# Performance work log

Measured on AMD Instinct MI355X. Metric: run time of the kernel, lower is better.

Reference implementation:

```python
import jax, jax.numpy as jnp
import numpy as np

N, XDIM, D, K = 400000, 128, 3, 4
TWO_PI = 2.0 * np.pi


def _scaled(k, shape):
    fan_in = shape[0]
    return jax.random.normal(k, shape, jnp.float32) * np.float32(1.0 / np.sqrt(fan_in))


def setup_inputs() -> dict:
    key = jax.random.key(0)
    ks = jax.random.split(key, 9)
    return {
        "x1": jax.random.normal(ks[0], (N, XDIM), jnp.float32),
        "enc_w1": _scaled(ks[1], (XDIM, 16)), "enc_b1": jnp.zeros((16,), jnp.float32),
        "enc_w2": _scaled(ks[2], (16, 8)),   "enc_b2": jnp.zeros((8,), jnp.float32),
        "enc_w3": _scaled(ks[3], (8, 1)),    "enc_b3": jnp.zeros((1,), jnp.float32),
        "dec_w1": _scaled(ks[4], (1, 8)),    "dec_b1": jnp.zeros((8,), jnp.float32),
        "dec_w2": _scaled(ks[5], (8, 16)),   "dec_b2": jnp.zeros((16,), jnp.float32),
        "dec_w3": _scaled(ks[6], (16, XDIM)),"dec_b3": jnp.zeros((XDIM,), jnp.float32),
        "est_w1": _scaled(ks[7], (D, 8)),    "est_b1": jnp.zeros((8,), jnp.float32),
        "est_w2": _scaled(ks[8], (8, K)),    "est_b2": jnp.zeros((K,), jnp.float32),
    }


def reference(x1, enc_w1, enc_b1, enc_w2, enc_b2, enc_w3, enc_b3,
              dec_w1, dec_b1, dec_w2, dec_b2, dec_w3, dec_b3,
              est_w1, est_b1, est_w2, est_b2):
    # encoder: Dense(16,tanh)->Dense(8,tanh)->Dense(1,tanh)
    h = jnp.tanh(x1 @ enc_w1 + enc_b1)
    h = jnp.tanh(h @ enc_w2 + enc_b2)
    z1 = jnp.tanh(h @ enc_w3 + enc_b3)            # [N,1]
    # decoder: Dense(8,tanh)->Dense(16,tanh)->Dense(xdim, linear)
    h = jnp.tanh(z1 @ dec_w1 + dec_b1)
    h = jnp.tanh(h @ dec_w2 + dec_b2)
    x2 = h @ dec_w3 + dec_b3                      # [N,xdim]

    # relative distances
    dist_cos = jnp.sum(x1 * x2, axis=1, keepdims=True) / (
        jnp.linalg.norm(x1, axis=1, keepdims=True) * jnp.linalg.norm(x2, axis=1, keepdims=True))
    dist_euc = jnp.linalg.norm(x1 - x2, axis=1, keepdims=True)
    z = jnp.concatenate([z1, dist_cos, dist_euc], axis=1)   # [N,D]

    # estimator: Dense(8,tanh)->Dense(K,softmax)
    gamma = jax.nn.softmax(jnp.tanh(z @ est_w1 + est_b1) @ est_w2 + est_b2)  # [N,K]

    # GMM parameters from soft assignments
    gamma_sum = jnp.sum(gamma, axis=0)                        # [K]
    phi = jnp.mean(gamma, axis=0)                             # [K]
    mu = jnp.einsum('ik,il->kl', gamma, z) / gamma_sum[:, None]          # [K,D]
    z_centered = jnp.sqrt(gamma)[:, :, None] * (z[:, None, :] - mu[None, :, :])  # [N,K,D]
    sigma = jnp.einsum('ikl,ikm->klm', z_centered, z_centered) / gamma_sum[:, None, None]  # [K,D,D]

    # per-sample energy
    z_mu = z[:, None, :] - mu[None, :, :]                     # [N,K,D]
    sigma_inv = jnp.linalg.inv(sigma)                         # [K,D,D]
    item1 = jnp.log(phi)[None, :]                             # [1,K]
    item2 = -0.5 * jnp.einsum('nkd,kde,nke->nk', z_mu, sigma_inv, z_mu)  # [N,K]
    sigma_det = jnp.linalg.det(TWO_PI * sigma)                # [K]
    item3 = jnp.log(jnp.sqrt(sigma_det))[None, :]             # [1,K]
    energy = -jnp.sum(item1 + item2 - item3, axis=1)          # [N]

    # loss
    lambda1, lambda2 = 0.01, 0.0001
    diag = jnp.diagonal(sigma, axis1=-2, axis2=-1)            # [K,D]
    loss3 = lambda2 * jnp.sum(1.0 / diag)
    loss2 = lambda1 * jnp.mean(energy)
    loss1 = jnp.mean(jnp.sum(jnp.square(x1 - x2), axis=1))
    loss = loss1 + loss2 + loss3
    return energy, loss
```

## Files before the change

kernel.cpp:

```cpp
#include <hip/hip_runtime.h>

#define NSAMP 400000
#define NBLK  1563


__device__ __forceinline__ float ftanh(float x) {
    float e = __expf(2.0f * x);
    return 1.0f - __fdividef(2.0f, e + 1.0f);
}

__global__ __launch_bounds__(256) void prep_kernel(const float* __restrict__ dw3,
                                                   const float* __restrict__ db3,
                                                   float* __restrict__ Gm,
                                                   float* __restrict__ gv,
                                                   float* __restrict__ bb) {
    __shared__ float sw3[2048];
    __shared__ float sb3[128];
    int t = threadIdx.x;
    for (int k = t; k < 2048; k += 256) sw3[k] = dw3[k];
    if (t < 128) sb3[t] = db3[t];
    __syncthreads();
    int a = t >> 4, b = t & 15;
    float s = 0.f;
    for (int j = 0; j < 128; ++j) s = fmaf(sw3[a * 128 + j], sw3[b * 128 + j], s);
    Gm[t] = s;
    if (t < 16) {
        float sg = 0.f;
        for (int j = 0; j < 128; ++j) sg = fmaf(sw3[t * 128 + j], sb3[j], sg);
        gv[t] = sg;
    }
    if (t == 0) {
        float sbv = 0.f;
        for (int j = 0; j < 128; ++j) sbv = fmaf(sb3[j], sb3[j], sbv);
        *bb = sbv;
    }
}

__global__ __launch_bounds__(256) void pass1_kernel(
    const float* __restrict__ x1,
    const float* __restrict__ ew1, const float* __restrict__ eb1,
    const float* __restrict__ ew2, const float* __restrict__ eb2,
    const float* __restrict__ ew3, const float* __restrict__ eb3,
    const float* __restrict__ dw1, const float* __restrict__ db1,
    const float* __restrict__ dw2, const float* __restrict__ db2,
    const float* __restrict__ dw3, const float* __restrict__ db3,
    const float* __restrict__ tw1, const float* __restrict__ tb1,
    const float* __restrict__ tw2, const float* __restrict__ tb2,
    const float* __restrict__ Gm, const float* __restrict__ gv,
    const float* __restrict__ bbp,
    double* __restrict__ acc, float4* __restrict__ zbuf) {
    __shared__ float4 lbuf[2048];
    __shared__ float sPart[4][41];
    __shared__ __align__(16) float sEw1[2048];
    __shared__ __align__(16) float sDw3[2048];
    __shared__ __align__(16) float sGm[256];
    __shared__ __align__(16) float sDb3[128];
    __shared__ __align__(16) float sEw2[128];
    __shared__ __align__(16) float sDw2[128];
    __shared__ __align__(16) float sTw1[24];
    __shared__ __align__(16) float sTw2[32];
    __shared__ float sGv[16], sEb1[16], sDb2[16];
    __shared__ float sEb2[8], sEw3[8], sDw1[8], sDb1[8], sTb1[8];
    __shared__ float sTb2[4];
    __shared__ float sBb, sEb3;

    int t = threadIdx.x;
    int i = blockIdx.x * 256 + t;
    bool active = (i < NSAMP);
    int bbase = blockIdx.x * 256;
    int w = t >> 6, lane = t & 63;
    int sw2 = (t >> 1) & 3;
    const float4* x1f4 = (const float4*)x1;

    const float4* p[4];
#pragma unroll
    for (int c2 = 0; c2 < 4; ++c2) {
        int idx = (w * 4 + c2) * 64 + lane;
        int row = idx >> 2, qs = idx & 3;
        int q = qs ^ ((row >> 1) & 3);
        int grow = bbase + row;
        if (grow >= NSAMP) grow = NSAMP - 1;
        p[c2] = x1f4 + (size_t)grow * 32 + q;
    }
#pragma unroll
    for (int c2 = 0; c2 < 4; ++c2) {
        __builtin_amdgcn_global_load_lds(
            (const __attribute__((address_space(1))) void*)p[c2],
            (__attribute__((address_space(3))) void*)(lbuf + (w * 4 + c2) * 64),
            16, 0, 0);
        p[c2] += 4;
    }

    for (int k = t; k < 2048; k += 256) { sEw1[k] = ew1[k]; sDw3[k] = dw3[k]; }
    sGm[t & 255] = Gm[t & 255];
    if (t < 128) { sDb3[t] = db3[t]; sEw2[t] = ew2[t]; sDw2[t] = dw2[t]; }
    if (t < 16) { sGv[t] = gv[t]; sEb1[t] = eb1[t]; sDb2[t] = db2[t]; }
    if (t < 8) { sEb2[t] = eb2[t]; sEw3[t] = ew3[t]; sDw1[t] = dw1[t];
                 sDb1[t] = db1[t]; sTb1[t] = tb1[t]; }
    if (t < 24) sTw1[t] = tw1[t];
    if (t < 32) sTw2[t] = tw2[t];
    if (t < 4) sTb2[t] = tb2[t];
    if (t == 0) { sBb = *bbp; sEb3 = eb3[0]; }
    __syncthreads();

    const float4* sEw1_4 = (const float4*)sEw1;
    const float4* sDw3_4 = (const float4*)sDw3;
    const float4* sDb3_4 = (const float4*)sDb3;
    const float4* sGm_4  = (const float4*)sGm;
    const float4* sEw2_4 = (const float4*)sEw2;
    const float4* sDw2_4 = (const float4*)sDw2;
    const float4* sTw1_4 = (const float4*)sTw1;
    const float4* sTw2_4 = (const float4*)sTw2;

    float u[16], v[16];
#pragma unroll
    for (int k = 0; k < 16; ++k) { u[k] = 0.f; v[k] = 0.f; }
    float s2 = 0.f, sb = 0.f;

    auto consume = [&](int blk, int bofs) {
        float xe[16];
#pragma unroll
        for (int q = 0; q < 4; ++q) {
            float4 w4 = lbuf[bofs + t * 4 + (q ^ sw2)];
            xe[q * 4 + 0] = w4.x; xe[q * 4 + 1] = w4.y;
            xe[q * 4 + 2] = w4.z; xe[q * 4 + 3] = w4.w;
        }
        int j0 = blk * 16;
#pragma unroll
        for (int ee = 0; ee < 4; ++ee) {
            float4 bv = sDb3_4[(j0 >> 2) + ee];
            s2 = fmaf(xe[ee*4+0], xe[ee*4+0], s2); sb = fmaf(xe[ee*4+0], bv.x, sb);
            s2 = fmaf(xe[ee*4+1], xe[ee*4+1], s2); sb = fmaf(xe[ee*4+1], bv.y, sb);
            s2 = fmaf(xe[ee*4+2], xe[ee*4+2], s2); sb = fmaf(xe[ee*4+2], bv.z, sb);
            s2 = fmaf(xe[ee*4+3], xe[ee*4+3], s2); sb = fmaf(xe[ee*4+3], bv.w, sb);
        }
#pragma unroll
        for (int e = 0; e < 16; ++e) {
            float x = xe[e];
#pragma unroll
            for (int kk = 0; kk < 4; ++kk) {
                float4 wv = sEw1_4[(j0 + e) * 4 + kk];
                u[kk*4+0] = fmaf(x, wv.x, u[kk*4+0]);
                u[kk*4+1] = fmaf(x, wv.y, u[kk*4+1]);
                u[kk*4+2] = fmaf(x, wv.z, u[kk*4+2]);
                u[kk*4+3] = fmaf(x, wv.w, u[kk*4+3]);
            }
        }
#pragma unroll
        for (int q = 0; q < 16; ++q) {
            float a2 = v[q];
#pragma unroll
            for (int ee = 0; ee < 4; ++ee) {
                float4 wv = sDw3_4[q * 32 + (j0 >> 2) + ee];
                a2 = fmaf(xe[ee*4+0], wv.x, a2);
                a2 = fmaf(xe[ee*4+1], wv.y, a2);
                a2 = fmaf(xe[ee*4+2], wv.z, a2);
                a2 = fmaf(xe[ee*4+3], wv.w, a2);
            }
            v[q] = a2;
        }
    };

#pragma unroll 1
    for (int blk = 0; blk < 7; ++blk) {
        int nb = ((blk + 1) & 1) * 1024;
#pragma unroll
        for (int c2 = 0; c2 < 4; ++c2) {
            __builtin_amdgcn_global_load_lds(
                (const __attribute__((address_space(1))) void*)p[c2],
                (__attribute__((address_space(3))) void*)(lbuf + nb + (w * 4 + c2) * 64),
                16, 0, 0);
            p[c2] += 4;
        }
        asm volatile("s_waitcnt vmcnt(4)" ::: "memory");
        __builtin_amdgcn_sched_barrier(0);
        consume(blk, (blk & 1) * 1024);
    }
    asm volatile("s_waitcnt vmcnt(0)" ::: "memory");
    __builtin_amdgcn_sched_barrier(0);
    consume(7, 1024);

    float h1[16];
#pragma unroll
    for (int k = 0; k < 16; ++k) h1[k] = ftanh(u[k] + sEb1[k]);
    float a2m[8];
#pragma unroll
    for (int m = 0; m < 8; ++m) a2m[m] = sEb2[m];
#pragma unroll
    for (int k = 0; k < 16; ++k) {
        float4 r0 = sEw2_4[k * 2], r1 = sEw2_4[k * 2 + 1];
        a2m[0] = fmaf(h1[k], r0.x, a2m[0]); a2m[1] = fmaf(h1[k], r0.y, a2m[1]);
        a2m[2] = fmaf(h1[k], r0.z, a2m[2]); a2m[3] = fmaf(h1[k], r0.w, a2m[3]);
        a2m[4] = fmaf(h1[k], r1.x, a2m[4]); a2m[5] = fmaf(h1[k], r1.y, a2m[5]);
        a2m[6] = fmaf(h1[k], r1.z, a2m[6]); a2m[7] = fmaf(h1[k], r1.w, a2m[7]);
    }
    float h2[8];
#pragma unroll
    for (int m = 0; m < 8; ++m) h2[m] = ftanh(a2m[m]);
    float a3 = sEb3;
#pragma unroll
    for (int m = 0; m < 8; ++m) a3 = fmaf(h2[m], sEw3[m], a3);
    float z1 = ftanh(a3);

    float d1[8];
#pragma unroll
    for (int p2 = 0; p2 < 8; ++p2) d1[p2] = ftanh(fmaf(z1, sDw1[p2], sDb1[p2]));
    float a2q[16];
#pragma unroll
    for (int q = 0; q < 16; ++q) a2q[q] = sDb2[q];
#pragma unroll
    for (int p2 = 0; p2 < 8; ++p2) {
#pragma unroll
        for (int q4 = 0; q4 < 4; ++q4) {
            float4 r = sDw2_4[p2 * 4 + q4];
            a2q[q4*4+0] = fmaf(d1[p2], r.x, a2q[q4*4+0]);
            a2q[q4*4+1] = fmaf(d1[p2], r.y, a2q[q4*4+1]);
            a2q[q4*4+2] = fmaf(d1[p2], r.z, a2q[q4*4+2]);
            a2q[q4*4+3] = fmaf(d1[p2], r.w, a2q[q4*4+3]);
        }
    }
    float d2[16];
#pragma unroll
    for (int q = 0; q < 16; ++q) d2[q] = ftanh(a2q[q]);

    float dot = sb;
#pragma unroll
    for (int q = 0; q < 16; ++q) dot = fmaf(d2[q], v[q], dot);
    float n2 = sBb;
#pragma unroll
    for (int a = 0; a < 16; ++a) {
        float ra = 2.0f * sGv[a];
#pragma unroll
        for (int b4 = 0; b4 < 4; ++b4) {
            float4 g = sGm_4[a * 4 + b4];
            ra = fmaf(g.x, d2[b4*4+0], ra);
            ra = fmaf(g.y, d2[b4*4+1], ra);
            ra = fmaf(g.z, d2[b4*4+2], ra);
            ra = fmaf(g.w, d2[b4*4+3], ra);
        }
        n2 = fmaf(d2[a], ra, n2);
    }
    n2 = fmaxf(n2, 1e-20f);
    float euc2 = fmaxf(s2 - 2.0f * dot + n2, 0.f);
    float deuc = sqrtf(euc2);
    float dcos = dot * rsqrtf(s2 * n2);

    float zf[3] = {z1, dcos, deuc};

    float e1a[8];
#pragma unroll
    for (int p2 = 0; p2 < 8; ++p2) e1a[p2] = sTb1[p2];
#pragma unroll
    for (int d = 0; d < 3; ++d) {
        float4 r0 = sTw1_4[d * 2], r1 = sTw1_4[d * 2 + 1];
        e1a[0] = fmaf(zf[d], r0.x, e1a[0]); e1a[1] = fmaf(zf[d], r0.y, e1a[1]);
        e1a[2] = fmaf(zf[d], r0.z, e1a[2]); e1a[3] = fmaf(zf[d], r0.w, e1a[3]);
        e1a[4] = fmaf(zf[d], r1.x, e1a[4]); e1a[5] = fmaf(zf[d], r1.y, e1a[5]);
        e1a[6] = fmaf(zf[d], r1.z, e1a[6]); e1a[7] = fmaf(zf[d], r1.w, e1a[7]);
    }
    float e1[8];
#pragma unroll
    for (int p2 = 0; p2 < 8; ++p2) e1[p2] = ftanh(e1a[p2]);
    float lg[4];
#pragma unroll
    for (int k = 0; k < 4; ++k) lg[k] = sTb2[k];
#pragma unroll
    for (int p2 = 0; p2 < 8; ++p2) {
        float4 r = sTw2_4[p2];
        lg[0] = fmaf(e1[p2], r.x, lg[0]); lg[1] = fmaf(e1[p2], r.y, lg[1]);
        lg[2] = fmaf(e1[p2], r.z, lg[2]); lg[3] = fmaf(e1[p2], r.w, lg[3]);
    }
    float mx = fmaxf(fmaxf(lg[0], lg[1]), fmaxf(lg[2], lg[3]));
    float ex[4]; float se = 0.f;
#pragma unroll
    for (int k = 0; k < 4; ++k) { ex[k] = __expf(lg[k] - mx); se += ex[k]; }
    float inv = __fdividef(1.0f, se);
    float gam[4];
#pragma unroll
    for (int k = 0; k < 4; ++k) gam[k] = ex[k] * inv;

    if (active) zbuf[i] = make_float4(zf[0], zf[1], zf[2], 0.f);
    if (!active) { gam[0] = gam[1] = gam[2] = gam[3] = 0.f; euc2 = 0.f; }

    int rlane = threadIdx.x & 63;
    int wid = threadIdx.x >> 6;

#define REDUCE_STORE(T, VAL) { float _v = (VAL);                          \
        _v += __shfl_down(_v, 32); _v += __shfl_down(_v, 16);             \
        _v += __shfl_down(_v, 8);  _v += __shfl_down(_v, 4);              \
        _v += __shfl_down(_v, 2);  _v += __shfl_down(_v, 1);              \
        if (rlane == 0) sPart[wid][T] = _v; }

#pragma unroll
    for (int k = 0; k < 4; ++k) REDUCE_STORE(k, gam[k]);
#pragma unroll
    for (int k = 0; k < 4; ++k) {
#pragma unroll
        for (int d = 0; d < 3; ++d) REDUCE_STORE(4 + k * 3 + d, gam[k] * zf[d]);
    }
#pragma unroll
    for (int k = 0; k < 4; ++k) {
        REDUCE_STORE(16 + k * 6 + 0, gam[k] * zf[0] * zf[0]);
        REDUCE_STORE(16 + k * 6 + 1, gam[k] * zf[0] * zf[1]);
        REDUCE_STORE(16 + k * 6 + 2, gam[k] * zf[0] * zf[2]);
        REDUCE_STORE(16 + k * 6 + 3, gam[k] * zf[1] * zf[1]);
        REDUCE_STORE(16 + k * 6 + 4, gam[k] * zf[1] * zf[2]);
        REDUCE_STORE(16 + k * 6 + 5, gam[k] * zf[2] * zf[2]);
    }
    REDUCE_STORE(40, euc2);
#undef REDUCE_STORE

    __syncthreads();
    if (threadIdx.x < 41) {
        double s = (double)sPart[0][threadIdx.x] + (double)sPart[1][threadIdx.x]
                 + (double)sPart[2][threadIdx.x] + (double)sPart[3][threadIdx.x];
        double* accs = acc + (size_t)(blockIdx.x & 7) * 48;
        unsafeAtomicAdd(&accs[threadIdx.x], s);
    }
}

__global__ void gmm_kernel(double* __restrict__ acc, float* __restrict__ P) {
    if (threadIdx.x != 0 || blockIdx.x != 0) return;
    for (int j = 0; j < 42; ++j) {
        double s = acc[j];
        for (int c = 1; c < 8; ++c) s += acc[c * 48 + j];
        acc[j] = s;
    }
    double M[6] = {0, 0, 0, 0, 0, 0}, bv[3] = {0, 0, 0}, A = 0.0, loss3 = 0.0;
    const double TWO_PI = 6.283185307179586;
    for (int k = 0; k < 4; ++k) {
        double g = acc[k];
        double phi = g / (double)NSAMP;
        double mu0 = acc[4 + k * 3 + 0] / g;
        double mu1 = acc[4 + k * 3 + 1] / g;
        double mu2 = acc[4 + k * 3 + 2] / g;
        double S00 = acc[16 + k * 6 + 0] / g - mu0 * mu0;
        double S01 = acc[16 + k * 6 + 1] / g - mu0 * mu1;
        double S02 = acc[16 + k * 6 + 2] / g - mu0 * mu2;
        double S11 = acc[16 + k * 6 + 3] / g - mu1 * mu1;
        double S12 = acc[16 + k * 6 + 4] / g - mu1 * mu2;
        double S22 = acc[16 + k * 6 + 5] / g - mu2 * mu2;
        double c00 = S11 * S22 - S12 * S12;
        double c01 = S02 * S12 - S01 * S22;
        double c02 = S01 * S12 - S02 * S11;
        double det = S00 * c00 + S01 * c01 + S02 * c02;
        double id = 1.0 / det;
        double I00 = c00 * id, I01 = c01 * id, I02 = c02 * id;
        double I11 = (S00 * S22 - S02 * S02) * id;
        double I12 = (S01 * S02 - S00 * S12) * id;
        double I22 = (S00 * S11 - S01 * S01) * id;
        M[0] += I00; M[1] += I01; M[2] += I02; M[3] += I11; M[4] += I12; M[5] += I22;
        double b0 = I00 * mu0 + I01 * mu1 + I02 * mu2;
        double b1 = I01 * mu0 + I11 * mu1 + I12 * mu2;
        double b2 = I02 * mu0 + I12 * mu1 + I22 * mu2;
        bv[0] += b0; bv[1] += b1; bv[2] += b2;
        double quad = mu0 * b0 + mu1 * b1 + mu2 * b2;
        A += -log(phi) + 0.5 * log(TWO_PI * TWO_PI * TWO_PI * det) + 0.5 * quad;
        loss3 += 1e-4 * (1.0 / S00 + 1.0 / S11 + 1.0 / S22);
    }
    P[0] = (float)M[0]; P[1] = (float)M[1]; P[2] = (float)M[2];
    P[3] = (float)M[3]; P[4] = (float)M[4]; P[5] = (float)M[5];
    P[6] = (float)bv[0]; P[7] = (float)bv[1]; P[8] = (float)bv[2];
    P[9] = (float)A;
    acc[42] = acc[40] / (double)NSAMP + loss3;
}

__global__ __launch_bounds__(256) void energy_kernel(const float4* __restrict__ zbuf,
                                                     const float* __restrict__ P,
                                                     double* __restrict__ acc,
                                                     unsigned* __restrict__ cnt,
                                                     float* __restrict__ out) {
    int i = blockIdx.x * 256 + threadIdx.x;
    float e = 0.f;
    if (i < NSAMP) {
        float4 z4 = zbuf[i];
        float z0 = z4.x, z1 = z4.y, z2 = z4.z;
        float q = P[0] * z0 * z0 + P[3] * z1 * z1 + P[5] * z2 * z2
                + 2.f * (P[1] * z0 * z1 + P[2] * z0 * z2 + P[4] * z1 * z2);
        e = P[9] + 0.5f * q - (P[6] * z0 + P[7] * z1 + P[8] * z2);
        out[i] = e;
    }
    float s = e;
    s += __shfl_down(s, 32); s += __shfl_down(s, 16); s += __shfl_down(s, 8);
    s += __shfl_down(s, 4);  s += __shfl_down(s, 2);  s += __shfl_down(s, 1);
    __shared__ float sE[4];
    if ((threadIdx.x & 63) == 0) sE[threadIdx.x >> 6] = s;
    __syncthreads();
    if (threadIdx.x == 0) {
        double t = (double)sE[0] + (double)sE[1] + (double)sE[2] + (double)sE[3];
        double* accs = acc + (size_t)(blockIdx.x & 7) * 48;
        unsafeAtomicAdd(&accs[41], t);
        __threadfence();
        unsigned old = atomicAdd(cnt, 1u);
        if (old == (unsigned)(NBLK - 1)) {
            double tot = 0.0;
            for (int c = 0; c < 8; ++c)
                tot += unsafeAtomicAdd(&acc[c * 48 + 41], 0.0);
            out[NSAMP] = (float)(acc[42] + 0.01 * tot / (double)NSAMP);
        }
    }
}

extern "C" void kernel_launch(void* const* d_in, const int* in_sizes, int n_in,
                              void* d_out, int out_size, void* d_ws, size_t ws_size,
                              hipStream_t stream) {
    const float* x1  = (const float*)d_in[0];
    const float* ew1 = (const float*)d_in[1];
    const float* eb1 = (const float*)d_in[2];
    const float* ew2 = (const float*)d_in[3];
    const float* eb2 = (const float*)d_in[4];
    const float* ew3 = (const float*)d_in[5];
    const float* eb3 = (const float*)d_in[6];
    const float* dw1 = (const float*)d_in[7];
    const float* db1 = (const float*)d_in[8];
    const float* dw2 = (const float*)d_in[9];
    const float* db2 = (const float*)d_in[10];
    const float* dw3 = (const float*)d_in[11];
    const float* db3 = (const float*)d_in[12];
    const float* tw1 = (const float*)d_in[13];
    const float* tb1 = (const float*)d_in[14];
    const float* tw2 = (const float*)d_in[15];
    const float* tb2 = (const float*)d_in[16];
    float* out = (float*)d_out;
    char* ws = (char*)d_ws;
    double* acc   = (double*)ws;
    unsigned* cnt = (unsigned*)(ws + 3072);
    float* P    = (float*)(ws + 3584);
    float* Gm   = (float*)(ws + 4096);
    float* gv   = (float*)(ws + 5120);
    float* bb   = (float*)(ws + 5184);
    float4* zb  = (float4*)(ws + 8192);

    hipMemsetAsync(d_ws, 0, 3584, stream);
    prep_kernel<<<1, 256, 0, stream>>>(dw3, db3, Gm, gv, bb);
    pass1_kernel<<<NBLK, 256, 0, stream>>>(x1, ew1, eb1, ew2, eb2, ew3, eb3,
                                           dw1, db1, dw2, db2, dw3, db3,
                                           tw1, tb1, tw2, tb2, Gm, gv, bb, acc, zb);
    gmm_kernel<<<1, 64, 0, stream>>>(acc, P);
    energy_kernel<<<NBLK, 256, 0, stream>>>(zb, P, acc, cnt, out);
}
```

Measured before the change: 456.7 us.

## Process two samples per thread in pass1 to reuse LDS weight loads

Each pass1 thread now computes two rows instead of one, so every LDS read of the encoder and decoder weights feeds FMAs for both samples. The grid is halved, x1 is streamed in 16 smaller double-buffered stages with a reworked swizzle, and the MLP tail is run once per row. Launch bounds request 3 blocks per CU. The extra accumulators roughly double register pressure, which could cause spills or lower occupancy, and there are fewer blocks to hide memory latency.

Result: slower. 667.8 us (+46.2%).

```diff
diff --git a/kernel.cpp b/kernel.cpp
--- a/kernel.cpp
+++ b/kernel.cpp
@@ -2,6 +2,7 @@
 
 #define NSAMP 400000
 #define NBLK  1563
+#define NBLKP 782
 
 
 __device__ __forceinline__ float ftanh(float x) {
@@ -36,7 +37,7 @@
     }
 }
 
-__global__ __launch_bounds__(256) void pass1_kernel(
+__global__ __launch_bounds__(256, 3) void pass1_kernel(
     const float* __restrict__ x1,
     const float* __restrict__ ew1, const float* __restrict__ eb1,
     const float* __restrict__ ew2, const float* __restrict__ eb2,
@@ -65,34 +66,35 @@
     __shared__ float sBb, sEb3;
 
     int t = threadIdx.x;
-    int i = blockIdx.x * 256 + t;
-    bool active = (i < NSAMP);
-    int bbase = blockIdx.x * 256;
+    int bbase = blockIdx.x * 512;
+    int ia = bbase + 2 * t, ib = ia + 1;
+    bool act_a = (ia < NSAMP), act_b = (ib < NSAMP);
     int w = t >> 6, lane = t & 63;
     int sw2 = (t >> 1) & 3;
     const float4* x1f4 = (const float4*)x1;
 
     const float4* p[4];
 #pragma unroll
-    for (int c2 = 0; c2 < 4; ++c2) {
-        int idx = (w * 4 + c2) * 64 + lane;
-        int row = idx >> 2, qs = idx & 3;
-        int q = qs ^ ((row >> 1) & 3);
+    for (int c = 0; c < 4; ++c) {
+        int S = w * 256 + c * 64 + lane;
+        int to = S >> 2, jp = S & 3;
+        int j = jp ^ ((to >> 1) & 3);
+        int row = 2 * to + (j >> 1), q = j & 1;
         int grow = bbase + row;
         if (grow >= NSAMP) grow = NSAMP - 1;
-        p[c2] = x1f4 + (size_t)grow * 32 + q;
-    }
-#pragma unroll
-    for (int c2 = 0; c2 < 4; ++c2) {
+        p[c] = x1f4 + (size_t)grow * 32 + q;
+    }
+#pragma unroll
+    for (int c = 0; c < 4; ++c) {
         __builtin_amdgcn_global_load_lds(
-            (const __attribute__((address_space(1))) void*)p[c2],
-            (__attribute__((address_space(3))) void*)(lbuf + (w * 4 + c2) * 64),
+            (const __attribute__((address_space(1))) void*)p[c],
+            (__attribute__((address_space(3))) void*)(lbuf + (w * 4 + c) * 64),
             16, 0, 0);
-        p[c2] += 4;
+        p[c] += 2;
     }
 
     for (int k = t; k < 2048; k += 256) { sEw1[k] = ew1[k]; sDw3[k] = dw3[k]; }
-    sGm[t & 255] = Gm[t & 255];
+    sGm[t] = Gm[t];
     if (t < 128) { sDb3[t] = db3[t]; sEw2[t] = ew2[t]; sDw2[t] = dw2[t]; }
     if (t < 16) { sGv[t] = gv[t]; sEb1[t] = eb1[t]; sDb2[t] = db2[t]; }
     if (t < 8) { sEb2[t] = eb2[t]; sEw3[t] = ew3[t]; sDw1[t] = dw1[t];
@@ -112,175 +114,181 @@
     const float4* sTw1_4 = (const float4*)sTw1;
     const float4* sTw2_4 = (const float4*)sTw2;
 
-    float u[16], v[16];
-#pragma unroll
-    for (int k = 0; k < 16; ++k) { u[k] = 0.f; v[k] = 0.f; }
-    float s2 = 0.f, sb = 0.f;
-
-    auto consume = [&](int blk, int bofs) {
-        float xe[16];
-#pragma unroll
-        for (int q = 0; q < 4; ++q) {
-            float4 w4 = lbuf[bofs + t * 4 + (q ^ sw2)];
-            xe[q * 4 + 0] = w4.x; xe[q * 4 + 1] = w4.y;
-            xe[q * 4 + 2] = w4.z; xe[q * 4 + 3] = w4.w;
-        }
-        int j0 = blk * 16;
-#pragma unroll
-        for (int ee = 0; ee < 4; ++ee) {
-            float4 bv = sDb3_4[(j0 >> 2) + ee];
-            s2 = fmaf(xe[ee*4+0], xe[ee*4+0], s2); sb = fmaf(xe[ee*4+0], bv.x, sb);
-            s2 = fmaf(xe[ee*4+1], xe[ee*4+1], s2); sb = fmaf(xe[ee*4+1], bv.y, sb);
-            s2 = fmaf(xe[ee*4+2], xe[ee*4+2], s2); sb = fmaf(xe[ee*4+2], bv.z, sb);
-            s2 = fmaf(xe[ee*4+3], xe[ee*4+3], s2); sb = fmaf(xe[ee*4+3], bv.w, sb);
-        }
-#pragma unroll
-        for (int e = 0; e < 16; ++e) {
-            float x = xe[e];
+    float ua[16], va[16], ub[16], vb[16];
+#pragma unroll
+    for (int k = 0; k < 16; ++k) { ua[k] = 0.f; va[k] = 0.f; ub[k] = 0.f; vb[k] = 0.f; }
+    float s2a = 0.f, sba = 0.f, s2b = 0.f, sbb = 0.f;
+
+    auto consume = [&](int s, int bofs) {
+        float4 w0 = lbuf[bofs + t * 4 + (0 ^ sw2)];
+        float4 w1 = lbuf[bofs + t * 4 + (1 ^ sw2)];
+        float4 w2 = lbuf[bofs + t * 4 + (2 ^ sw2)];
+        float4 w3 = lbuf[bofs + t * 4 + (3 ^ sw2)];
+        float xa[8] = {w0.x, w0.y, w0.z, w0.w, w1.x, w1.y, w1.z, w1.w};
+        float xb[8] = {w2.x, w2.y, w2.z, w2.w, w3.x, w3.y, w3.z, w3.w};
+        float4 b0 = sDb3_4[s * 2], b1 = sDb3_4[s * 2 + 1];
+        float bx[8] = {b0.x, b0.y, b0.z, b0.w, b1.x, b1.y, b1.z, b1.w};
+#pragma unroll
+        for (int e = 0; e < 8; ++e) {
+            s2a = fmaf(xa[e], xa[e], s2a); sba = fmaf(xa[e], bx[e], sba);
+            s2b = fmaf(xb[e], xb[e], s2b); sbb = fmaf(xb[e], bx[e], sbb);
+        }
+#pragma unroll
+        for (int e = 0; e < 8; ++e) {
+            int jr = s * 8 + e;
 #pragma unroll
             for (int kk = 0; kk < 4; ++kk) {
-                float4 wv = sEw1_4[(j0 + e) * 4 + kk];
-                u[kk*4+0] = fmaf(x, wv.x, u[kk*4+0]);
-                u[kk*4+1] = fmaf(x, wv.y, u[kk*4+1]);
-                u[kk*4+2] = fmaf(x, wv.z, u[kk*4+2]);
-                u[kk*4+3] = fmaf(x, wv.w, u[kk*4+3]);
+                float4 wv = sEw1_4[jr * 4 + kk];
+                ua[kk*4+0] = fmaf(xa[e], wv.x, ua[kk*4+0]);
+                ua[kk*4+1] = fmaf(xa[e], wv.y, ua[kk*4+1]);
+                ua[kk*4+2] = fmaf(xa[e], wv.z, ua[kk*4+2]);
+                ua[kk*4+3] = fmaf(xa[e], wv.w, ua[kk*4+3]);
+                ub[kk*4+0] = fmaf(xb[e], wv.x, ub[kk*4+0]);
+                ub[kk*4+1] = fmaf(xb[e], wv.y, ub[kk*4+1]);
+                ub[kk*4+2] = fmaf(xb[e], wv.z, ub[kk*4+2]);
+                ub[kk*4+3] = fmaf(xb[e], wv.w, ub[kk*4+3]);
             }
         }
 #pragma unroll
         for (int q = 0; q < 16; ++q) {
-            float a2 = v[q];
-#pragma unroll
-            for (int ee = 0; ee < 4; ++ee) {
-                float4 wv = sDw3_4[q * 32 + (j0 >> 2) + ee];
-                a2 = fmaf(xe[ee*4+0], wv.x, a2);
-                a2 = fmaf(xe[ee*4+1], wv.y, a2);
-                a2 = fmaf(xe[ee*4+2], wv.z, a2);
-                a2 = fmaf(xe[ee*4+3], wv.w, a2);
+            float aa = va[q], ab = vb[q];
+#pragma unroll
+            for (int ee = 0; ee < 2; ++ee) {
+                float4 wv = sDw3_4[q * 32 + s * 2 + ee];
+                aa = fmaf(xa[ee*4+0], wv.x, aa); aa = fmaf(xa[ee*4+1], wv.y, aa);
+                aa = fmaf(xa[ee*4+2], wv.z, aa); aa = fmaf(xa[ee*4+3], wv.w, aa);
+                ab = fmaf(xb[ee*4+0], wv.x, ab); ab = fmaf(xb[ee*4+1], wv.y, ab);
+                ab = fmaf(xb[ee*4+2], wv.z, ab); ab = fmaf(xb[ee*4+3], wv.w, ab);
             }
-            v[q] = a2;
+            va[q] = aa; vb[q] = ab;
         }
     };
 
 #pragma unroll 1
-    for (int blk = 0; blk < 7; ++blk) {
-        int nb = ((blk + 1) & 1) * 1024;
-#pragma unroll
-        for (int c2 = 0; c2 < 4; ++c2) {
+    for (int s = 0; s < 15; ++s) {
+        int nb = ((s + 1) & 1) * 1024;
+#pragma unroll
+        for (int c = 0; c < 4; ++c) {
             __builtin_amdgcn_global_load_lds(
-                (const __attribute__((address_space(1))) void*)p[c2],
-                (__attribute__((address_space(3))) void*)(lbuf + nb + (w * 4 + c2) * 64),
+                (const __attribute__((address_space(1))) void*)p[c],
+                (__attribute__((address_space(3))) void*)(lbuf + nb + (w * 4 + c) * 64),
                 16, 0, 0);
-            p[c2] += 4;
+            p[c] += 2;
         }
         asm volatile("s_waitcnt vmcnt(4)" ::: "memory");
         __builtin_amdgcn_sched_barrier(0);
-        consume(blk, (blk & 1) * 1024);
+        consume(s, (s & 1) * 1024);
     }
     asm volatile("s_waitcnt vmcnt(0)" ::: "memory");
     __builtin_amdgcn_sched_barrier(0);
-    consume(7, 1024);
-
-    float h1[16];
-#pragma unroll
-    for (int k = 0; k < 16; ++k) h1[k] = ftanh(u[k] + sEb1[k]);
-    float a2m[8];
-#pragma unroll
-    for (int m = 0; m < 8; ++m) a2m[m] = sEb2[m];
-#pragma unroll
-    for (int k = 0; k < 16; ++k) {
-        float4 r0 = sEw2_4[k * 2], r1 = sEw2_4[k * 2 + 1];
-        a2m[0] = fmaf(h1[k], r0.x, a2m[0]); a2m[1] = fmaf(h1[k], r0.y, a2m[1]);
-        a2m[2] = fmaf(h1[k], r0.z, a2m[2]); a2m[3] = fmaf(h1[k], r0.w, a2m[3]);
-        a2m[4] = fmaf(h1[k], r1.x, a2m[4]); a2m[5] = fmaf(h1[k], r1.y, a2m[5]);
-        a2m[6] = fmaf(h1[k], r1.z, a2m[6]); a2m[7] = fmaf(h1[k], r1.w, a2m[7]);
-    }
-    float h2[8];
-#pragma unroll
-    for (int m = 0; m < 8; ++m) h2[m] = ftanh(a2m[m]);
-    float a3 = sEb3;
-#pragma unroll
-    for (int m = 0; m < 8; ++m) a3 = fmaf(h2[m], sEw3[m], a3);
-    float z1 = ftanh(a3);
-
-    float d1[8];
-#pragma unroll
-    for (int p2 = 0; p2 < 8; ++p2) d1[p2] = ftanh(fmaf(z1, sDw1[p2], sDb1[p2]));
-    float a2q[16];
-#pragma unroll
-    for (int q = 0; q < 16; ++q) a2q[q] = sDb2[q];
-#pragma unroll
-    for (int p2 = 0; p2 < 8; ++p2) {
-#pragma unroll
-        for (int q4 = 0; q4 < 4; ++q4) {
-            float4 r = sDw2_4[p2 * 4 + q4];
-            a2q[q4*4+0] = fmaf(d1[p2], r.x, a2q[q4*4+0]);
-            a2q[q4*4+1] = fmaf(d1[p2], r.y, a2q[q4*4+1]);
-            a2q[q4*4+2] = fmaf(d1[p2], r.z, a2q[q4*4+2]);
-            a2q[q4*4+3] = fmaf(d1[p2], r.w, a2q[q4*4+3]);
-        }
-    }
-    float d2[16];
-#pragma unroll
-    for (int q = 0; q < 16; ++q) d2[q] = ftanh(a2q[q]);
-
-    float dot = sb;
-#pragma unroll
-    for (int q = 0; q < 16; ++q) dot = fmaf(d2[q], v[q], dot);
-    float n2 = sBb;
-#pragma unroll
-    for (int a = 0; a < 16; ++a) {
-        float ra = 2.0f * sGv[a];
-#pragma unroll
-        for (int b4 = 0; b4 < 4; ++b4) {
-            float4 g = sGm_4[a * 4 + b4];
-            ra = fmaf(g.x, d2[b4*4+0], ra);
-            ra = fmaf(g.y, d2[b4*4+1], ra);
-            ra = fmaf(g.z, d2[b4*4+2], ra);
-            ra = fmaf(g.w, d2[b4*4+3], ra);
-        }
-        n2 = fmaf(d2[a], ra, n2);
-    }
-    n2 = fmaxf(n2, 1e-20f);
-    float euc2 = fmaxf(s2 - 2.0f * dot + n2, 0.f);
-    float deuc = sqrtf(euc2);
-    float dcos = dot * rsqrtf(s2 * n2);
-
-    float zf[3] = {z1, dcos, deuc};
-
-    float e1a[8];
-#pragma unroll
-    for (int p2 = 0; p2 < 8; ++p2) e1a[p2] = sTb1[p2];
-#pragma unroll
-    for (int d = 0; d < 3; ++d) {
-        float4 r0 = sTw1_4[d * 2], r1 = sTw1_4[d * 2 + 1];
-        e1a[0] = fmaf(zf[d], r0.x, e1a[0]); e1a[1] = fmaf(zf[d], r0.y, e1a[1]);
-        e1a[2] = fmaf(zf[d], r0.z, e1a[2]); e1a[3] = fmaf(zf[d], r0.w, e1a[3]);
-        e1a[4] = fmaf(zf[d], r1.x, e1a[4]); e1a[5] = fmaf(zf[d], r1.y, e1a[5]);
-        e1a[6] = fmaf(zf[d], r1.z, e1a[6]); e1a[7] = fmaf(zf[d], r1.w, e1a[7]);
-    }
-    float e1[8];
-#pragma unroll
-    for (int p2 = 0; p2 < 8; ++p2) e1[p2] = ftanh(e1a[p2]);
-    float lg[4];
-#pragma unroll
-    for (int k = 0; k < 4; ++k) lg[k] = sTb2[k];
-#pragma unroll
-    for (int p2 = 0; p2 < 8; ++p2) {
-        float4 r = sTw2_4[p2];
-        lg[0] = fmaf(e1[p2], r.x, lg[0]); lg[1] = fmaf(e1[p2], r.y, lg[1]);
-        lg[2] = fmaf(e1[p2], r.z, lg[2]); lg[3] = fmaf(e1[p2], r.w, lg[3]);
-    }
-    float mx = fmaxf(fmaxf(lg[0], lg[1]), fmaxf(lg[2], lg[3]));
-    float ex[4]; float se = 0.f;
-#pragma unroll
-    for (int k = 0; k < 4; ++k) { ex[k] = __expf(lg[k] - mx); se += ex[k]; }
-    float inv = __fdividef(1.0f, se);
-    float gam[4];
-#pragma unroll
-    for (int k = 0; k < 4; ++k) gam[k] = ex[k] * inv;
-
-    if (active) zbuf[i] = make_float4(zf[0], zf[1], zf[2], 0.f);
-    if (!active) { gam[0] = gam[1] = gam[2] = gam[3] = 0.f; euc2 = 0.f; }
+    consume(15, 1024);
+
+    auto tail = [&](float (&u)[16], float (&v)[16], float s2, float sb,
+                    float (&zf)[3], float (&gam)[4], float &euc2) {
+        float h1[16];
+#pragma unroll
+        for (int k = 0; k < 16; ++k) h1[k] = ftanh(u[k] + sEb1[k]);
+        float a2m[8];
+#pragma unroll
+        for (int m = 0; m < 8; ++m) a2m[m] = sEb2[m];
+#pragma unroll
+        for (int k = 0; k < 16; ++k) {
+            float4 r0 = sEw2_4[k * 2], r1 = sEw2_4[k * 2 + 1];
+            a2m[0] = fmaf(h1[k], r0.x, a2m[0]); a2m[1] = fmaf(h1[k], r0.y, a2m[1]);
+            a2m[2] = fmaf(h1[k], r0.z, a2m[2]); a2m[3] = fmaf(h1[k], r0.w, a2m[3]);
+            a2m[4] = fmaf(h1[k], r1.x, a2m[4]); a2m[5] = fmaf(h1[k], r1.y, a2m[5]);
+            a2m[6] = fmaf(h1[k], r1.z, a2m[6]); a2m[7] = fmaf(h1[k], r1.w, a2m[7]);
+        }
+        float h2[8];
+#pragma unroll
+        for (int m = 0; m < 8; ++m) h2[m] = ftanh(a2m[m]);
+        float a3 = sEb3;
+#pragma unroll
+        for (int m = 0; m < 8; ++m) a3 = fmaf(h2[m], sEw3[m], a3);
+        float z1 = ftanh(a3);
+        float d1[8];
+#pragma unroll
+        for (int p2 = 0; p2 < 8; ++p2) d1[p2] = ftanh(fmaf(z1, sDw1[p2], sDb1[p2]));
+        float a2q[16];
+#pragma unroll
+        for (int q = 0; q < 16; ++q) a2q[q] = sDb2[q];
+#pragma unroll
+        for (int p2 = 0; p2 < 8; ++p2) {
+#pragma unroll
+            for (int q4 = 0; q4 < 4; ++q4) {
+                float4 r = sDw2_4[p2 * 4 + q4];
+                a2q[q4*4+0] = fmaf(d1[p2], r.x, a2q[q4*4+0]);
+                a2q[q4*4+1] = fmaf(d1[p2], r.y, a2q[q4*4+1]);
+                a2q[q4*4+2] = fmaf(d1[p2], r.z, a2q[q4*4+2]);
+                a2q[q4*4+3] = fmaf(d1[p2], r.w, a2q[q4*4+3]);
+            }
+        }
+        float d2[16];
+#pragma unroll
+        for (int q = 0; q < 16; ++q) d2[q] = ftanh(a2q[q]);
+        float dot = sb;
+#pragma unroll
+        for (int q = 0; q < 16; ++q) dot = fmaf(d2[q], v[q], dot);
+        float n2 = sBb;
+#pragma unroll
+        for (int a = 0; a < 16; ++a) {
+            float ra = 2.0f * sGv[a];
+#pragma unroll
+            for (int b4 = 0; b4 < 4; ++b4) {
+                float4 g = sGm_4[a * 4 + b4];
+                ra = fmaf(g.x, d2[b4*4+0], ra);
+                ra = fmaf(g.y, d2[b4*4+1], ra);
+                ra = fmaf(g.z, d2[b4*4+2], ra);
+                ra = fmaf(g.w, d2[b4*4+3], ra);
+            }
+            n2 = fmaf(d2[a], ra, n2);
+        }
+        n2 = fmaxf(n2, 1e-20f);
+        euc2 = fmaxf(s2 - 2.0f * dot + n2, 0.f);
+        float deuc = sqrtf(euc2);
+        float dcos = dot * rsqrtf(s2 * n2);
+        zf[0] = z1; zf[1] = dcos; zf[2] = deuc;
+        float e1a[8];
+#pragma unroll
+        for (int p2 = 0; p2 < 8; ++p2) e1a[p2] = sTb1[p2];
+#pragma unroll
+        for (int d = 0; d < 3; ++d) {
+            float4 r0 = sTw1_4[d * 2], r1 = sTw1_4[d * 2 + 1];
+            e1a[0] = fmaf(zf[d], r0.x, e1a[0]); e1a[1] = fmaf(zf[d], r0.y, e1a[1]);
+            e1a[2] = fmaf(zf[d], r0.z, e1a[2]); e1a[3] = fmaf(zf[d], r0.w, e1a[3]);
+            e1a[4] = fmaf(zf[d], r1.x, e1a[4]); e1a[5] = fmaf(zf[d], r1.y, e1a[5]);
+            e1a[6] = fmaf(zf[d], r1.z, e1a[6]); e1a[7] = fmaf(zf[d], r1.w, e1a[7]);
+        }
+        float e1[8];
+#pragma unroll
+        for (int p2 = 0; p2 < 8; ++p2) e1[p2] = ftanh(e1a[p2]);
+        float lg[4];
+#pragma unroll
+        for (int k = 0; k < 4; ++k) lg[k] = sTb2[k];
+#pragma unroll
+        for (int p2 = 0; p2 < 8; ++p2) {
+            float4 r = sTw2_4[p2];
+            lg[0] = fmaf(e1[p2], r.x, lg[0]); lg[1] = fmaf(e1[p2], r.y, lg[1]);
+            lg[2] = fmaf(e1[p2], r.z, lg[2]); lg[3] = fmaf(e1[p2], r.w, lg[3]);
+        }
+        float mx = fmaxf(fmaxf(lg[0], lg[1]), fmaxf(lg[2], lg[3]));
+        float ex[4]; float se = 0.f;
+#pragma unroll
+        for (int k = 0; k < 4; ++k) { ex[k] = __expf(lg[k] - mx); se += ex[k]; }
+        float inv = __fdividef(1.0f, se);
+#pragma unroll
+        for (int k = 0; k < 4; ++k) gam[k] = ex[k] * inv;
+    };
+
+    float zfa[3], gama[4], euc2a;
+    float zfb[3], gamb[4], euc2b;
+    tail(ua, va, s2a, sba, zfa, gama, euc2a);
+    tail(ub, vb, s2b, sbb, zfb, gamb, euc2b);
+
+    if (act_a) zbuf[ia] = make_float4(zfa[0], zfa[1], zfa[2], 0.f);
+    if (act_b) zbuf[ib] = make_float4(zfb[0], zfb[1], zfb[2], 0.f);
+    if (!act_a) { gama[0] = gama[1] = gama[2] = gama[3] = 0.f; euc2a = 0.f; }
+    if (!act_b) { gamb[0] = gamb[1] = gamb[2] = gamb[3] = 0.f; euc2b = 0.f; }
 
     int rlane = threadIdx.x & 63;
     int wid = threadIdx.x >> 6;
@@ -292,22 +300,23 @@
         if (rlane == 0) sPart[wid][T] = _v; }
 
 #pragma unroll
-    for (int k = 0; k < 4; ++k) REDUCE_STORE(k, gam[k]);
+    for (int k = 0; k < 4; ++k) REDUCE_STORE(k, gama[k] + gamb[k]);
 #pragma unroll
     for (int k = 0; k < 4; ++k) {
 #pragma unroll
-        for (int d = 0; d < 3; ++d) REDUCE_STORE(4 + k * 3 + d, gam[k] * zf[d]);
+        for (int d = 0; d < 3; ++d)
+            REDUCE_STORE(4 + k * 3 + d, gama[k] * zfa[d] + gamb[k] * zfb[d]);
     }
 #pragma unroll
     for (int k = 0; k < 4; ++k) {
-        REDUCE_STORE(16 + k * 6 + 0, gam[k] * zf[0] * zf[0]);
-        REDUCE_STORE(16 + k * 6 + 1, gam[k] * zf[0] * zf[1]);
-        REDUCE_STORE(16 + k * 6 + 2, gam[k] * zf[0] * zf[2]);
-        REDUCE_STORE(16 + k * 6 + 3, gam[k] * zf[1] * zf[1]);
-        REDUCE_STORE(16 + k * 6 + 4, gam[k] * zf[1] * zf[2]);
-        REDUCE_STORE(16 + k * 6 + 5, gam[k] * zf[2] * zf[2]);
-    }
-    REDUCE_STORE(40, euc2);
+        REDUCE_STORE(16 + k * 6 + 0, gama[k]*zfa[0]*zfa[0] + gamb[k]*zfb[0]*zfb[0]);
+        REDUCE_STORE(16 + k * 6 + 1, gama[k]*zfa[0]*zfa[1] + gamb[k]*zfb[0]*zfb[1]);
+        REDUCE_STORE(16 + k * 6 + 2, gama[k]*zfa[0]*zfa[2] + gamb[k]*zfb[0]*zfb[2]);
+        REDUCE_STORE(16 + k * 6 + 3, gama[k]*zfa[1]*zfa[1] + gamb[k]*zfb[1]*zfb[1]);
+        REDUCE_STORE(16 + k * 6 + 4, gama[k]*zfa[1]*zfa[2] + gamb[k]*zfb[1]*zfb[2]);
+        REDUCE_STORE(16 + k * 6 + 5, gama[k]*zfa[2]*zfa[2] + gamb[k]*zfb[2]*zfb[2]);
+    }
+    REDUCE_STORE(40, euc2a + euc2b);
 #undef REDUCE_STORE
 
     __syncthreads();
@@ -433,9 +442,9 @@
 
     hipMemsetAsync(d_ws, 0, 3584, stream);
     prep_kernel<<<1, 256, 0, stream>>>(dw3, db3, Gm, gv, bb);
-    pass1_kernel<<<NBLK, 256, 0, stream>>>(x1, ew1, eb1, ew2, eb2, ew3, eb3,
-                                           dw1, db1, dw2, db2, dw3, db3,
-                                           tw1, tb1, tw2, tb2, Gm, gv, bb, acc, zb);
+    pass1_kernel<<<NBLKP, 256, 0, stream>>>(x1, ew1, eb1, ew2, eb2, ew3, eb3,
+                                            dw1, db1, dw2, db2, dw3, db3,
+                                            tw1, tb1, tw2, tb2, Gm, gv, bb, acc, zb);
     gmm_kernel<<<1, 64, 0, stream>>>(acc, P);
     energy_kernel<<<NBLK, 256, 0, stream>>>(zb, P, acc, cnt, out);
 }
```
